# Performance work log

Measured on AMD Instinct MI355X. Metric: run time of the kernel, lower is better.

## Reference

```python
import math
import jax, jax.numpy as jnp
import numpy as np

K = 2                 # top-k gate
CAP_FACTOR = 1.0      # capacity_factor
EPS = 1e-9


def setup_inputs() -> dict:
    key = jax.random.key(0)
    ks = jax.random.split(key, 6)
    B, S, D, H, E = 4, 2048, 1024, 4096, 8
    x = jax.random.normal(ks[0], (B, S, D), jnp.float32)
    wg = jax.random.normal(ks[1], (D, E), jnp.float32) * 0.02
    w1 = jax.random.normal(ks[2], (E, D, H), jnp.float32) * 0.02
    b1 = jnp.zeros((E, H), jnp.float32)
    w2 = jax.random.normal(ks[3], (E, H, D), jnp.float32) * 0.02
    b2 = jnp.zeros((E, D), jnp.float32)
    return {"x": x, "wg": wg, "w1": w1, "b1": b1, "w2": w2, "b2": b2}


def reference(x, wg, w1, b1, w2, b2):
    B, S, D = x.shape
    E = wg.shape[1]
    xt = x.reshape(-1, D)                      # [N, D] tokens
    N = xt.shape[0]
    cap = int(math.ceil(CAP_FACTOR * K * N / E))

    # fp32 gate: softmax scores, top-k selection, normalized gates
    logits = xt.astype(jnp.float32) @ wg.astype(jnp.float32)    # [N, E]
    scores = jax.nn.softmax(logits, axis=-1)
    gvals, gidx = jax.lax.top_k(scores, K)                      # [N, K]
    gvals = gvals / jnp.clip(gvals.sum(-1, keepdims=True), EPS)

    # GShard-style capacity locations: k-th choice offset by earlier choices' counts
    offset = jnp.zeros((E,), jnp.int32)
    pos_l, keep_l = [], []
    for kk in range(K):
        m = jax.nn.one_hot(gidx[:, kk], E, dtype=jnp.int32)     # [N, E]
        loc = jnp.cumsum(m, axis=0) - 1 + offset[None, :]
        offset = offset + m.sum(axis=0)
        pos = jnp.take_along_axis(loc, gidx[:, kk:kk + 1], axis=1)[:, 0]
        keep = pos < cap
        pos_l.append(jnp.where(keep, pos, 0))
        keep_l.append(keep)
    pos = jnp.stack(pos_l, axis=1)             # [N, K]
    keep = jnp.stack(keep_l, axis=1)           # [N, K] bool
    gvals = gvals * keep                       # drop overflowed tokens

    e_flat = gidx.reshape(-1)                  # [N*K]
    p_flat = pos.reshape(-1)
    kmask = keep.reshape(-1).astype(x.dtype)
    x_rep = jnp.repeat(xt, K, axis=0)          # [N*K, D], token-major matches reshape

    # dispatch (scatter to expert slots); postscore=True -> no gate weight here
    disp = jnp.zeros((E, cap, D), x.dtype).at[e_flat, p_flat].add(x_rep * kmask[:, None])

    # grouped expert FFN with exact GELU
    h = jax.nn.gelu(jnp.einsum('ecd,edh->ech', disp, w1) + b1[:, None, :], approximate=False)
    y = jnp.einsum('ech,ehd->ecd', h, w2) + b2[:, None, :]      # [E, cap, D]

    # combine (gather + gate-weighted sum over k)
    yk = y[e_flat, p_flat]                                      # [N*K, D]
    w = gvals.reshape(-1).astype(x.dtype)
    out = (yk * w[:, None]).reshape(N, K, D).sum(axis=1)
    return out.reshape(B, S, D)
```

## Files before the change

### kernel.cpp

```cpp
#include <hip/hip_runtime.h>
#include <hip/hip_bf16.h>
#include <math.h>

#define N_TOK 8192
#define DIM   1024
#define HID   4096
#define NEXP  8
#define CAP   2048

typedef short bf16x8 __attribute__((ext_vector_type(8)));
typedef float f32x4  __attribute__((ext_vector_type(4)));

__device__ __forceinline__ unsigned short f2bf(float f) {
    union { float f; unsigned u; } v; v.f = f;
    unsigned r = v.u;
    unsigned lsb = (r >> 16) & 1u;
    r += 0x7fffu + lsb;
    return (unsigned short)(r >> 16);
}

__global__ __launch_bounds__(256) void init_kernel(float* __restrict__ out,
                                                   int* __restrict__ slot_token,
                                                   float* __restrict__ slot_gate) {
    int gid = blockIdx.x * 256 + threadIdx.x;
    f32x4 z = {0.f, 0.f, 0.f, 0.f};
    *(f32x4*)(out + (size_t)gid * 4) = z;
    if (gid < NEXP * CAP) { slot_token[gid] = -1; slot_gate[gid] = 0.f; }
}

__global__ __launch_bounds__(256) void transpose_convert_kernel(
        const float* __restrict__ in, unsigned short* __restrict__ outp,
        int R, int C) {
    int e  = blockIdx.z;
    int c0 = blockIdx.x * 32, r0 = blockIdx.y * 32;
    __shared__ float tile[32][33];
    const float* ip = in + (size_t)e * R * C;
    unsigned short* op = outp + (size_t)e * R * C;
    int t = threadIdx.x;
    int tc = t & 31, tr = t >> 5;
    #pragma unroll
    for (int p = 0; p < 4; ++p) {
        int r = tr + p * 8;
        tile[r][tc] = ip[(size_t)(r0 + r) * C + c0 + tc];
    }
    __syncthreads();
    #pragma unroll
    for (int p = 0; p < 4; ++p) {
        int c = tr + p * 8;
        op[(size_t)(c0 + c) * R + r0 + tc] = f2bf(tile[tc][c]);
    }
}

__global__ __launch_bounds__(256) void gate_kernel(
        const float* __restrict__ x, const float* __restrict__ wg,
        int* __restrict__ tok_e, float* __restrict__ tok_g) {
    int wave = threadIdx.x >> 6, lane = threadIdx.x & 63;
    int n = blockIdx.x * 4 + wave;
    const float* xr = x + (size_t)n * DIM;
    float acc[8];
    #pragma unroll
    for (int e = 0; e < 8; ++e) acc[e] = 0.f;
    for (int j = 0; j < DIM / 64; ++j) {
        int d = lane + 64 * j;
        float xv = xr[d];
        const f32x4* wr = (const f32x4*)(wg + (size_t)d * 8);
        f32x4 w0 = wr[0], w1 = wr[1];
        acc[0] += xv * w0[0]; acc[1] += xv * w0[1];
        acc[2] += xv * w0[2]; acc[3] += xv * w0[3];
        acc[4] += xv * w1[0]; acc[5] += xv * w1[1];
        acc[6] += xv * w1[2]; acc[7] += xv * w1[3];
    }
    #pragma unroll
    for (int off = 32; off > 0; off >>= 1) {
        #pragma unroll
        for (int e = 0; e < 8; ++e) acc[e] += __shfl_down(acc[e], off);
    }
    if (lane == 0) {
        float mx = acc[0];
        #pragma unroll
        for (int e = 1; e < 8; ++e) mx = fmaxf(mx, acc[e]);
        float p[8], s = 0.f;
        #pragma unroll
        for (int e = 0; e < 8; ++e) { p[e] = expf(acc[e] - mx); s += p[e]; }
        int i0 = 0;
        #pragma unroll
        for (int e = 1; e < 8; ++e) if (acc[e] > acc[i0]) i0 = e;
        int i1 = (i0 == 0) ? 1 : 0;
        #pragma unroll
        for (int e = 0; e < 8; ++e) if (e != i0 && acc[e] > acc[i1]) i1 = e;
        float g0 = p[i0] / s, g1 = p[i1] / s;
        float gs = fmaxf(g0 + g1, 1e-9f);
        tok_e[n * 2 + 0] = i0;  tok_e[n * 2 + 1] = i1;
        tok_g[n * 2 + 0] = g0 / gs;  tok_g[n * 2 + 1] = g1 / gs;
    }
}

__global__ __launch_bounds__(512) void route_kernel(
        const int* __restrict__ tok_e, const float* __restrict__ tok_g,
        int* __restrict__ slot_token, float* __restrict__ slot_gate) {
    __shared__ int te[N_TOK];
    int w = threadIdx.x >> 6;
    int lane = threadIdx.x & 63;
    unsigned long long below = (lane == 63) ? 0x7fffffffffffffffull
                                            : ((1ull << lane) - 1ull);
    int cnt = 0;
    for (int kk = 0; kk < 2; ++kk) {
        __syncthreads();
        for (int i = threadIdx.x; i < N_TOK; i += 512) te[i] = tok_e[i * 2 + kk];
        __syncthreads();
        #pragma unroll 4
        for (int base = 0; base < N_TOK; base += 64) {
            int n = base + lane;
            bool mine = (te[n] == w);
            unsigned long long m = __ballot(mine);
            if (mine) {
                int pos = cnt + __popcll(m & below);
                if (pos < CAP) {
                    slot_token[w * CAP + pos] = n;
                    slot_gate[w * CAP + pos]  = tok_g[n * 2 + kk];
                }
            }
            cnt += __popcll(m);
        }
    }
}

__global__ __launch_bounds__(256) void dispatch_kernel(
        const float* __restrict__ x, const int* __restrict__ slot_token,
        unsigned short* __restrict__ disp) {
    int s = blockIdx.x;
    int tok = slot_token[s];
    int t = threadIdx.x;
    unsigned short* dp = disp + (size_t)s * DIM + t * 4;
    uint2 o;
    if (tok < 0) { o.x = 0u; o.y = 0u; }
    else {
        const f32x4 v = *(const f32x4*)(x + (size_t)tok * DIM + t * 4);
        o.x = (unsigned)f2bf(v[0]) | ((unsigned)f2bf(v[1]) << 16);
        o.y = (unsigned)f2bf(v[2]) | ((unsigned)f2bf(v[3]) << 16);
    }
    *(uint2*)dp = o;
}

template<int KD>
__device__ __forceinline__ void mainloop256(
        const unsigned short* __restrict__ Ag, const unsigned short* __restrict__ Bg,
        unsigned short* lds, f32x4 (&acc)[8][4]) {
    const int t = threadIdx.x;
    const int w = t >> 6, l = t & 63;
    const int wm = w >> 2, wn = w & 3;

    const int slot0 = w * 64 + l;
    const int slot1 = 512 + w * 64 + l;
    const int r0 = (slot0 >> 6) * 16 + (slot0 & 15), c0 = (slot0 >> 4) & 3;
    const int r1 = (slot1 >> 6) * 16 + (slot1 & 15), c1 = (slot1 >> 4) & 3;
    const size_t ofs0 = (size_t)r0 * KD + c0 * 8;
    const size_t ofs1 = (size_t)r1 * KD + c1 * 8;
    const int dst0 = (w * 64) * 8;
    const int dst1 = (512 + w * 64) * 8;

    auto stage = [&](const unsigned short* G, int ldsbase, int kh, int kt) {
        __builtin_amdgcn_global_load_lds(
            (const __attribute__((address_space(1))) void*)(G + ofs0 + kt + kh * 32),
            (__attribute__((address_space(3))) void*)(lds + ldsbase + kh * 8192 + dst0), 16, 0, 0);
        __builtin_amdgcn_global_load_lds(
            (const __attribute__((address_space(1))) void*)(G + ofs1 + kt + kh * 32),
            (__attribute__((address_space(3))) void*)(lds + ldsbase + kh * 8192 + dst1), 16, 0, 0);
    };
    auto ldA = [&](int abase, int ks, int m) {
        return *(const bf16x8*)(lds + abase + ks * 8192 + (wm * 8 + m) * 512 + l * 8);
    };
    auto ldB = [&](int bbase, int ks, int n) {
        return *(const bf16x8*)(lds + bbase + ks * 8192 + (wn * 4 + n) * 512 + l * 8);
    };

#define MFMA_PAIR(nlo)                                                                     \
    __builtin_amdgcn_s_setprio(1);                                                         \
    _Pragma("unroll")                                                                      \
    for (int m = 0; m < 8; ++m) {                                                          \
        acc[m][nlo]     = __builtin_amdgcn_mfma_f32_16x16x32_bf16(af[m], bf[nlo],     acc[m][nlo],     0, 0, 0); \
        acc[m][nlo + 1] = __builtin_amdgcn_mfma_f32_16x16x32_bf16(af[m], bf[nlo + 1], acc[m][nlo + 1], 0, 0, 0); \
    }                                                                                      \
    __builtin_amdgcn_s_setprio(0);

    constexpr int NT = KD / 64;
    bf16x8 af[8], bf[4];

    stage(Ag, 0, 0, 0);  stage(Bg, 16384, 0, 0);
    stage(Ag, 0, 1, 0);  stage(Bg, 16384, 1, 0);

    int cur = 0;
#pragma unroll 1
    for (int T = 0; T < NT; ++T, cur ^= 1) {
        const int abase = cur * 32768, bbase = abase + 16384;
        const int nA = (cur ^ 1) * 32768, nB = nA + 16384;
        const int ktn = (T + 1) * 64;
        const bool pf = (T + 1 < NT);

        asm volatile("s_waitcnt vmcnt(4)\n\ts_barrier" ::: "memory");
        #pragma unroll
        for (int m = 0; m < 8; ++m) af[m] = ldA(abase, 0, m);
        bf[0] = ldB(bbase, 0, 0);  bf[1] = ldB(bbase, 0, 1);
        if (pf) stage(Ag, nA, 0, ktn);
        MFMA_PAIR(0)
        bf[2] = ldB(bbase, 0, 2);  bf[3] = ldB(bbase, 0, 3);
        if (pf) stage(Bg, nB, 0, ktn);
        MFMA_PAIR(2)
        if (pf) { asm volatile("s_waitcnt vmcnt(4)\n\ts_barrier" ::: "memory"); }
        else    { asm volatile("s_waitcnt vmcnt(0)\n\ts_barrier" ::: "memory"); }
        #pragma unroll
        for (int m = 0; m < 8; ++m) af[m] = ldA(abase, 1, m);
        bf[0] = ldB(bbase, 1, 0);  bf[1] = ldB(bbase, 1, 1);
        if (pf) stage(Ag, nA, 1, ktn);
        MFMA_PAIR(0)
        bf[2] = ldB(bbase, 1, 2);  bf[3] = ldB(bbase, 1, 3);
        if (pf) stage(Bg, nB, 1, ktn);
        MFMA_PAIR(2)
    }
#undef MFMA_PAIR
}

__global__ __launch_bounds__(512, 2) void gemm1_kernel(
        const unsigned short* __restrict__ disp, const unsigned short* __restrict__ w1t,
        const float* __restrict__ b1, unsigned short* __restrict__ h) {
    extern __shared__ unsigned short lds[];
    constexpr int TOT = (CAP / 256) * (HID / 256) * NEXP;
    constexpr int TPE = (CAP / 256) * (HID / 256);
    constexpr int TN  = HID / 256;
    const int bid = (blockIdx.x & 7) * (TOT >> 3) + (blockIdx.x >> 3);
    const int e = bid / TPE, tt = bid % TPE, tm = tt / TN, tn = tt % TN;

    const unsigned short* A = disp + ((size_t)e * CAP + tm * 256) * DIM;
    const unsigned short* B = w1t  + ((size_t)e * HID + tn * 256) * DIM;
    f32x4 acc[8][4];
    #pragma unroll
    for (int m = 0; m < 8; ++m)
        #pragma unroll
        for (int n = 0; n < 4; ++n) acc[m][n] = (f32x4){0.f, 0.f, 0.f, 0.f};

    mainloop256<DIM>(A, B, lds, acc);

    const int l = threadIdx.x & 63, w = threadIdx.x >> 6;
    const int l16 = l & 15, kh4 = l >> 4;
    const int wm = w >> 2, wn = w & 3;
    const float* b1e = b1 + (size_t)e * HID + tn * 256;
    float bias[4];
    #pragma unroll
    for (int n = 0; n < 4; ++n) bias[n] = b1e[wn * 64 + n * 16 + l16];
    unsigned short* H = h + ((size_t)e * CAP + tm * 256) * HID + tn * 256;
    #pragma unroll
    for (int m = 0; m < 8; ++m)
        #pragma unroll
        for (int n = 0; n < 4; ++n)
            #pragma unroll
            for (int r = 0; r < 4; ++r) {
                int row = wm * 128 + m * 16 + kh4 * 4 + r;
                int col = wn * 64 + n * 16 + l16;
                float v = acc[m][n][r] + bias[n];
                v = 0.5f * v * (1.0f + erff(v * 0.70710678118654752f));
                H[(size_t)row * HID + col] = f2bf(v);
            }
}

__global__ __launch_bounds__(512, 2) void gemm2_kernel(
        const unsigned short* __restrict__ h, const unsigned short* __restrict__ w2t,
        const float* __restrict__ b2, const int* __restrict__ slot_token,
        const float* __restrict__ slot_gate, float* __restrict__ out) {
    extern __shared__ unsigned short lds[];
    constexpr int TOT = (CAP / 256) * (DIM / 256) * NEXP;
    constexpr int TPE = (CAP / 256) * (DIM / 256);
    constexpr int TN  = DIM / 256;
    const int bid = (blockIdx.x & 7) * (TOT >> 3) + (blockIdx.x >> 3);
    const int e = bid / TPE, tt = bid % TPE, tm = tt / TN, tn = tt % TN;

    const unsigned short* A = h   + ((size_t)e * CAP + tm * 256) * HID;
    const unsigned short* B = w2t + ((size_t)e * DIM + tn * 256) * HID;
    f32x4 acc[8][4];
    #pragma unroll
    for (int m = 0; m < 8; ++m)
        #pragma unroll
        for (int n = 0; n < 4; ++n) acc[m][n] = (f32x4){0.f, 0.f, 0.f, 0.f};

    mainloop256<HID>(A, B, lds, acc);

    const int l = threadIdx.x & 63, w = threadIdx.x >> 6;
    const int l16 = l & 15, kh4 = l >> 4;
    const int wm = w >> 2, wn = w & 3;
    const float* b2e = b2 + (size_t)e * DIM + tn * 256;
    float bias[4];
    #pragma unroll
    for (int n = 0; n < 4; ++n) bias[n] = b2e[wn * 64 + n * 16 + l16];
    #pragma unroll
    for (int m = 0; m < 8; ++m)
        #pragma unroll
        for (int r = 0; r < 4; ++r) {
            int row = wm * 128 + m * 16 + kh4 * 4 + r;
            int slot = e * CAP + tm * 256 + row;
            int tok = slot_token[slot];
            if (tok >= 0) {
                float g = slot_gate[slot];
                #pragma unroll
                for (int n = 0; n < 4; ++n) {
                    int col = wn * 64 + n * 16 + l16;
                    float v = acc[m][n][r] + bias[n];
                    atomicAdd(out + (size_t)tok * DIM + tn * 256 + col, v * g);
                }
            }
        }
}

extern "C" void kernel_launch(void* const* d_in, const int* in_sizes, int n_in,
                              void* d_out, int out_size, void* d_ws, size_t ws_size,
                              hipStream_t stream) {
    (void)in_sizes; (void)n_in; (void)out_size; (void)ws_size;
    const float* x  = (const float*)d_in[0];
    const float* wg = (const float*)d_in[1];
    const float* w1 = (const float*)d_in[2];
    const float* b1 = (const float*)d_in[3];
    const float* w2 = (const float*)d_in[4];
    const float* b2 = (const float*)d_in[5];
    float* out = (float*)d_out;

    char* ws = (char*)d_ws;
    size_t off = 0;
    unsigned short* w1t  = (unsigned short*)(ws + off); off += (size_t)NEXP * HID * DIM * 2;
    unsigned short* w2t  = (unsigned short*)(ws + off); off += (size_t)NEXP * DIM * HID * 2;
    unsigned short* disp = (unsigned short*)(ws + off); off += (size_t)NEXP * CAP * DIM * 2;
    unsigned short* hbuf = (unsigned short*)(ws + off); off += (size_t)NEXP * CAP * HID * 2;
    int*   slot_token = (int*)  (ws + off); off += (size_t)NEXP * CAP * 4;
    float* slot_gate  = (float*)(ws + off); off += (size_t)NEXP * CAP * 4;
    int*   tok_e      = (int*)  (ws + off); off += (size_t)N_TOK * 2 * 4;
    float* tok_g      = (float*)(ws + off); off += (size_t)N_TOK * 2 * 4;

    hipFuncSetAttribute((const void*)gemm1_kernel,
                        hipFuncAttributeMaxDynamicSharedMemorySize, 131072);
    hipFuncSetAttribute((const void*)gemm2_kernel,
                        hipFuncAttributeMaxDynamicSharedMemorySize, 131072);

    hipLaunchKernelGGL(init_kernel, dim3(N_TOK * DIM / 4 / 256), dim3(256), 0, stream,
                       out, slot_token, slot_gate);
    hipLaunchKernelGGL(transpose_convert_kernel, dim3(HID / 32, DIM / 32, NEXP), dim3(256), 0, stream,
                       w1, w1t, DIM, HID);
    hipLaunchKernelGGL(transpose_convert_kernel, dim3(DIM / 32, HID / 32, NEXP), dim3(256), 0, stream,
                       w2, w2t, HID, DIM);
    hipLaunchKernelGGL(gate_kernel, dim3(N_TOK / 4), dim3(256), 0, stream, x, wg, tok_e, tok_g);
    hipLaunchKernelGGL(route_kernel, dim3(1), dim3(512), 0, stream,
                       tok_e, tok_g, slot_token, slot_gate);
    hipLaunchKernelGGL(dispatch_kernel, dim3(NEXP * CAP), dim3(256), 0, stream,
                       x, slot_token, disp);
    hipLaunchKernelGGL(gemm1_kernel, dim3((CAP / 256) * (HID / 256) * NEXP), dim3(512), 131072, stream,
                       disp, w1t, b1, hbuf);
    hipLaunchKernelGGL(gemm2_kernel, dim3((CAP / 256) * (DIM / 256) * NEXP), dim3(512), 131072, stream,
                       hbuf, w2t, b2, slot_token, slot_gate, out);
}
```

Baseline: 821.0 us.

## Replace atomic scatter-combine with dense expert output plus gather combine kernel

gemm2 now writes dense per-slot fp32 outputs into a buffer that reuses the w1t workspace, which is free by then. A new combine kernel gathers each token's two slots and applies the gate weights. This removes the fp32 atomics and the full zeroing of the output. The weight transpose-convert also moves to 64x64 tiles with vectorized loads and stores, and the exact erff GELU is replaced by an Abramowitz-Stegun polynomial approximation, which adds small numeric error.

After: 709.9 us. -13.5%, faster.

```diff
diff --git a/kernel.cpp b/kernel.cpp
--- a/kernel.cpp
+++ b/kernel.cpp
@@ -19,35 +19,52 @@
     return (unsigned short)(r >> 16);
 }
 
-__global__ __launch_bounds__(256) void init_kernel(float* __restrict__ out,
-                                                   int* __restrict__ slot_token,
-                                                   float* __restrict__ slot_gate) {
+__device__ __forceinline__ float gelu_f(float v) {
+    float az = fabsf(v);
+    float z  = az * 0.70710678118654752f;
+    float t  = __builtin_amdgcn_rcpf(fmaf(0.3275911f, z, 1.0f));
+    float p  = fmaf(fmaf(fmaf(fmaf(1.061405429f, t, -1.453152027f),
+                               t, 1.421413741f), t, -0.284496736f), t, 0.254829592f) * t;
+    float ez = __expf(-z * z);
+    float q5 = 0.5f * p * ez;
+    float phi = (v >= 0.f) ? (1.f - q5) : q5;
+    return v * phi;
+}
+
+__global__ __launch_bounds__(256) void init_kernel(int* __restrict__ slot_token) {
     int gid = blockIdx.x * 256 + threadIdx.x;
-    f32x4 z = {0.f, 0.f, 0.f, 0.f};
-    *(f32x4*)(out + (size_t)gid * 4) = z;
-    if (gid < NEXP * CAP) { slot_token[gid] = -1; slot_gate[gid] = 0.f; }
+    slot_token[gid] = -1;
 }
 
 __global__ __launch_bounds__(256) void transpose_convert_kernel(
         const float* __restrict__ in, unsigned short* __restrict__ outp,
         int R, int C) {
     int e  = blockIdx.z;
-    int c0 = blockIdx.x * 32, r0 = blockIdx.y * 32;
-    __shared__ float tile[32][33];
+    int c0 = blockIdx.x * 64, r0 = blockIdx.y * 64;
+    __shared__ float tile[64][65];
     const float* ip = in + (size_t)e * R * C;
     unsigned short* op = outp + (size_t)e * R * C;
     int t = threadIdx.x;
-    int tc = t & 31, tr = t >> 5;
+    int rr = t >> 4, cc = (t & 15) * 4;
     #pragma unroll
     for (int p = 0; p < 4; ++p) {
-        int r = tr + p * 8;
-        tile[r][tc] = ip[(size_t)(r0 + r) * C + c0 + tc];
+        f32x4 v = *(const f32x4*)(ip + (size_t)(r0 + p * 16 + rr) * C + c0 + cc);
+        tile[p * 16 + rr][cc + 0] = v[0];
+        tile[p * 16 + rr][cc + 1] = v[1];
+        tile[p * 16 + rr][cc + 2] = v[2];
+        tile[p * 16 + rr][cc + 3] = v[3];
     }
     __syncthreads();
+    int ct = t >> 4, rq = (t & 15) * 4;
     #pragma unroll
     for (int p = 0; p < 4; ++p) {
-        int c = tr + p * 8;
-        op[(size_t)(c0 + c) * R + r0 + tc] = f2bf(tile[tc][c]);
+        int c = p * 16 + ct;
+        ushort4 o;
+        o.x = f2bf(tile[rq + 0][c]);
+        o.y = f2bf(tile[rq + 1][c]);
+        o.z = f2bf(tile[rq + 2][c]);
+        o.w = f2bf(tile[rq + 3][c]);
+        *(ushort4*)(op + (size_t)(c0 + c) * R + r0 + rq) = o;
     }
 }
 
@@ -96,8 +113,8 @@
 }
 
 __global__ __launch_bounds__(512) void route_kernel(
-        const int* __restrict__ tok_e, const float* __restrict__ tok_g,
-        int* __restrict__ slot_token, float* __restrict__ slot_gate) {
+        const int* __restrict__ tok_e,
+        int* __restrict__ slot_token, int* __restrict__ tok_slot) {
     __shared__ int te[N_TOK];
     int w = threadIdx.x >> 6;
     int lane = threadIdx.x & 63;
@@ -115,10 +132,9 @@
             unsigned long long m = __ballot(mine);
             if (mine) {
                 int pos = cnt + __popcll(m & below);
-                if (pos < CAP) {
-                    slot_token[w * CAP + pos] = n;
-                    slot_gate[w * CAP + pos]  = tok_g[n * 2 + kk];
-                }
+                bool ok = pos < CAP;
+                tok_slot[n * 2 + kk] = ok ? (w * CAP + pos) : -1;
+                if (ok) slot_token[w * CAP + pos] = n;
             }
             cnt += __popcll(m);
         }
@@ -256,16 +272,13 @@
             for (int r = 0; r < 4; ++r) {
                 int row = wm * 128 + m * 16 + kh4 * 4 + r;
                 int col = wn * 64 + n * 16 + l16;
-                float v = acc[m][n][r] + bias[n];
-                v = 0.5f * v * (1.0f + erff(v * 0.70710678118654752f));
-                H[(size_t)row * HID + col] = f2bf(v);
+                H[(size_t)row * HID + col] = f2bf(gelu_f(acc[m][n][r] + bias[n]));
             }
 }
 
 __global__ __launch_bounds__(512, 2) void gemm2_kernel(
         const unsigned short* __restrict__ h, const unsigned short* __restrict__ w2t,
-        const float* __restrict__ b2, const int* __restrict__ slot_token,
-        const float* __restrict__ slot_gate, float* __restrict__ out) {
+        const float* __restrict__ b2, float* __restrict__ y) {
     extern __shared__ unsigned short lds[];
     constexpr int TOT = (CAP / 256) * (DIM / 256) * NEXP;
     constexpr int TPE = (CAP / 256) * (DIM / 256);
@@ -290,23 +303,35 @@
     float bias[4];
     #pragma unroll
     for (int n = 0; n < 4; ++n) bias[n] = b2e[wn * 64 + n * 16 + l16];
+    float* Y = y + ((size_t)e * CAP + tm * 256) * DIM + tn * 256;
     #pragma unroll
     for (int m = 0; m < 8; ++m)
         #pragma unroll
-        for (int r = 0; r < 4; ++r) {
-            int row = wm * 128 + m * 16 + kh4 * 4 + r;
-            int slot = e * CAP + tm * 256 + row;
-            int tok = slot_token[slot];
-            if (tok >= 0) {
-                float g = slot_gate[slot];
-                #pragma unroll
-                for (int n = 0; n < 4; ++n) {
-                    int col = wn * 64 + n * 16 + l16;
-                    float v = acc[m][n][r] + bias[n];
-                    atomicAdd(out + (size_t)tok * DIM + tn * 256 + col, v * g);
-                }
+        for (int n = 0; n < 4; ++n)
+            #pragma unroll
+            for (int r = 0; r < 4; ++r) {
+                int row = wm * 128 + m * 16 + kh4 * 4 + r;
+                int col = wn * 64 + n * 16 + l16;
+                Y[(size_t)row * DIM + col] = acc[m][n][r] + bias[n];
             }
-        }
+}
+
+__global__ __launch_bounds__(256) void combine_kernel(
+        const float* __restrict__ y, const int* __restrict__ tok_slot,
+        const float* __restrict__ tok_g, float* __restrict__ out) {
+    int n = blockIdx.x, t = threadIdx.x;
+    int s0 = tok_slot[n * 2], s1 = tok_slot[n * 2 + 1];
+    float g0 = tok_g[n * 2], g1 = tok_g[n * 2 + 1];
+    f32x4 r = {0.f, 0.f, 0.f, 0.f};
+    if (s0 >= 0) {
+        f32x4 v = *(const f32x4*)(y + (size_t)s0 * DIM + t * 4);
+        r[0] = g0 * v[0]; r[1] = g0 * v[1]; r[2] = g0 * v[2]; r[3] = g0 * v[3];
+    }
+    if (s1 >= 0) {
+        f32x4 v = *(const f32x4*)(y + (size_t)s1 * DIM + t * 4);
+        r[0] += g1 * v[0]; r[1] += g1 * v[1]; r[2] += g1 * v[2]; r[3] += g1 * v[3];
+    }
+    *(f32x4*)(out + (size_t)n * DIM + t * 4) = r;
 }
 
 extern "C" void kernel_launch(void* const* d_in, const int* in_sizes, int n_in,
@@ -328,28 +353,31 @@
     unsigned short* disp = (unsigned short*)(ws + off); off += (size_t)NEXP * CAP * DIM * 2;
     unsigned short* hbuf = (unsigned short*)(ws + off); off += (size_t)NEXP * CAP * HID * 2;
     int*   slot_token = (int*)  (ws + off); off += (size_t)NEXP * CAP * 4;
-    float* slot_gate  = (float*)(ws + off); off += (size_t)NEXP * CAP * 4;
     int*   tok_e      = (int*)  (ws + off); off += (size_t)N_TOK * 2 * 4;
     float* tok_g      = (float*)(ws + off); off += (size_t)N_TOK * 2 * 4;
+    int*   tok_slot   = (int*)  (ws + off); off += (size_t)N_TOK * 2 * 4;
+    float* ybuf = (float*)w1t;
 
     hipFuncSetAttribute((const void*)gemm1_kernel,
                         hipFuncAttributeMaxDynamicSharedMemorySize, 131072);
     hipFuncSetAttribute((const void*)gemm2_kernel,
                         hipFuncAttributeMaxDynamicSharedMemorySize, 131072);
 
-    hipLaunchKernelGGL(init_kernel, dim3(N_TOK * DIM / 4 / 256), dim3(256), 0, stream,
-                       out, slot_token, slot_gate);
-    hipLaunchKernelGGL(transpose_convert_kernel, dim3(HID / 32, DIM / 32, NEXP), dim3(256), 0, stream,
+    hipLaunchKernelGGL(init_kernel, dim3(NEXP * CAP / 256), dim3(256), 0, stream,
+                       slot_token);
+    hipLaunchKernelGGL(transpose_convert_kernel, dim3(HID / 64, DIM / 64, NEXP), dim3(256), 0, stream,
                        w1, w1t, DIM, HID);
-    hipLaunchKernelGGL(transpose_convert_kernel, dim3(DIM / 32, HID / 32, NEXP), dim3(256), 0, stream,
+    hipLaunchKernelGGL(transpose_convert_kernel, dim3(DIM / 64, HID / 64, NEXP), dim3(256), 0, stream,
                        w2, w2t, HID, DIM);
     hipLaunchKernelGGL(gate_kernel, dim3(N_TOK / 4), dim3(256), 0, stream, x, wg, tok_e, tok_g);
     hipLaunchKernelGGL(route_kernel, dim3(1), dim3(512), 0, stream,
-                       tok_e, tok_g, slot_token, slot_gate);
+                       tok_e, slot_token, tok_slot);
     hipLaunchKernelGGL(dispatch_kernel, dim3(NEXP * CAP), dim3(256), 0, stream,
                        x, slot_token, disp);
     hipLaunchKernelGGL(gemm1_kernel, dim3((CAP / 256) * (HID / 256) * NEXP), dim3(512), 131072, stream,
                        disp, w1t, b1, hbuf);
     hipLaunchKernelGGL(gemm2_kernel, dim3((CAP / 256) * (DIM / 256) * NEXP), dim3(512), 131072, stream,
-                       hbuf, w2t, b2, slot_token, slot_gate, out);
-}
+                       hbuf, w2t, b2, ybuf);
+    hipLaunchKernelGGL(combine_kernel, dim3(N_TOK), dim3(256), 0, stream,
+                       ybuf, tok_slot, tok_g, out);
+}
```
